# Kernel tuning notes

Hardware: AMD Instinct MI355X
Metric: run time of the kernel (lower is better)

The kernel has to match this reference:

```python
import jax, jax.numpy as jnp
import numpy as np

N_QUBITS = 8
N_LAYERS = 2
DIM = 2 ** N_QUBITS  # 256


def _ry(theta):
    h = theta * 0.5
    c, s = jnp.cos(h), jnp.sin(h)
    return jnp.stack([jnp.stack([c, -s]), jnp.stack([s, c])]).astype(jnp.complex64)


def _rz(theta):
    e = jnp.exp(-0.5j * theta.astype(jnp.complex64))
    z = jnp.zeros((), jnp.complex64)
    return jnp.stack([jnp.stack([e, z]), jnp.stack([z, jnp.conj(e)])])


def _apply_1q(state, U, w):
    # state: (2,)*n tensor, wire 0 = most significant (PennyLane convention)
    s = jnp.moveaxis(state, w, 0)
    s = jnp.tensordot(U, s, axes=((1,), (0,)))
    return jnp.moveaxis(s, 0, w)


def _cnot(state, c, t):
    s = jnp.moveaxis(state, (c, t), (0, 1))
    s = jnp.stack([s[0, 0], s[0, 1], s[1, 1], s[1, 0]]).reshape((2, 2) + s.shape[2:])
    return jnp.moveaxis(s, (0, 1), (c, t))


def _conv_pair(state, q1, q2, p):
    state = _apply_1q(state, _ry(p[0]), q1)
    state = _apply_1q(state, _ry(p[1]), q2)
    state = _cnot(state, q1, q2)
    state = _apply_1q(state, _ry(p[2]), q1)
    state = _apply_1q(state, _ry(p[3]), q2)
    state = _cnot(state, q2, q1)
    return state


def _circuit(angles, node_idx, adj, qp):
    n = N_QUBITS
    state = jnp.zeros((2,) * n, jnp.complex64).at[(0,) * n].set(1.0)
    a = jnp.clip(angles, -np.pi, np.pi)
    # angle encoding: RY on all wires, RZ on wires 0..n/2-1
    for i in range(n):
        state = _apply_1q(state, _ry(a[i]), i)
    for i in range(n // 2):
        state = _apply_1q(state, _rz(a[i + n // 2]), i)
    # graph-structure entanglement: conditional CNOT(c=node%n, t) if adj[c,t]>0
    c = (node_idx % n).astype(jnp.int32)
    adj_row = adj[c]
    flat = state.reshape(-1)
    idx = jnp.arange(DIM, dtype=jnp.int32)
    bit_c = (idx >> (n - 1 - c)) & 1  # dynamic control wire
    for t in range(n):
        perm = idx ^ (bit_c << (n - 1 - t))
        cond = (adj_row[t] > 0) & (t != c)
        flat = jnp.where(cond, flat[perm], flat)
    state = flat.reshape((2,) * n)
    # quantum conv layers
    ppc = 4 * (n - 1)
    off = 0
    for _ in range(N_LAYERS):
        p = qp[off:off + ppc]
        k = 0
        for i in range(0, n - 1, 2):
            state = _conv_pair(state, i, i + 1, p[k:k + 4]); k += 4
        for i in range(1, n - 1, 2):
            state = _conv_pair(state, i, i + 1, p[k:k + 4]); k += 4
        off += ppc
    # pooling rotations on even wires
    pool = qp[off:off + n]
    for q in range(0, n, 2):
        state = _apply_1q(state, _ry(pool[q]), q)
    # <Z_w> expectation values
    probs = jnp.abs(state) ** 2
    z = jnp.stack([probs.take(0, axis=w).sum() - probs.take(1, axis=w).sum()
                   for w in range(n)])
    return z


def setup_inputs() -> dict:
    key = jax.random.key(0)
    ks = jax.random.split(key, 12)
    B, S, N, F = 64, 12, 207, 2
    x = jax.random.normal(ks[0], (B, S, N, F), jnp.float32)
    adj = jax.random.randint(ks[1], (N, N), 0, 2).astype(jnp.float32)
    w_proj = jax.random.normal(ks[2], (N_QUBITS, S * F), jnp.float32) * 0.1
    b_proj = jax.random.normal(ks[3], (N_QUBITS,), jnp.float32) * 0.1
    q_params = jax.random.normal(ks[4], (4 * (N_QUBITS - 1) * N_LAYERS + N_QUBITS,), jnp.float32) * 0.1
    w1 = jax.random.normal(ks[5], (64, N_QUBITS), jnp.float32) * 0.1
    b1 = jax.random.normal(ks[6], (64,), jnp.float32) * 0.1
    w2 = jax.random.normal(ks[7], (32, 64), jnp.float32) * 0.1
    b2 = jax.random.normal(ks[8], (32,), jnp.float32) * 0.1
    w3 = jax.random.normal(ks[9], (1, 32), jnp.float32) * 0.1
    b3 = jax.random.normal(ks[10], (1,), jnp.float32) * 0.1
    return dict(x=x, adj=adj, w_proj=w_proj, b_proj=b_proj, q_params=q_params,
                w1=w1, b1=b1, w2=w2, b2=b2, w3=w3, b3=b3)


def reference(x, adj, w_proj, b_proj, q_params, w1, b1, w2, b2, w3, b3):
    B, S, N, F = x.shape
    feats = jnp.transpose(x, (0, 2, 1, 3)).reshape(B, N, S * F)
    angles = feats @ w_proj.T + b_proj                      # (B, N, 8)
    node_idx = jnp.tile(jnp.arange(N, dtype=jnp.int32), B)  # (B*N,)
    z = jax.vmap(_circuit, in_axes=(0, 0, None, None))(
        angles.reshape(B * N, N_QUBITS), node_idx, adj, q_params)
    # original detaches quantum features before the classical head
    z = jax.lax.stop_gradient(z).reshape(B, N, N_QUBITS).astype(jnp.float32)
    h = jax.nn.relu(z @ w1.T + b1)   # dropout is identity in eval mode
    h = jax.nn.relu(h @ w2.T + b2)
    out = h @ w3.T + b3              # (B, N, 1)
    return out.squeeze(-1)
```

## Files before the change

kernel.cpp:

```cpp
#include <hip/hip_runtime.h>
#include <math.h>

#define DEV static __device__ __forceinline__

constexpr int SS = 12;
constexpr int NN = 207;
constexpr int NCIRC = 64 * NN;


typedef float v2f __attribute__((ext_vector_type(2)));

DEV v2f splat2(float x) { v2f r; r.x = x; r.y = x; return r; }
DEV v2f vfma(float m, v2f a, v2f acc) { return __builtin_elementwise_fma(splat2(m), a, acc); }
DEV v2f vmul(float m, v2f a) { return splat2(m) * a; }
template<int M> DEV float sxc(float v) { return __shfl_xor(v, M, 64); }
template<int M> DEV v2f sx2(v2f v) { v2f r; r.x = sxc<M>(v.x); r.y = sxc<M>(v.y); return r; }

#define CONVM(P) do {                                                     \
    v2f _a0 = c0, _a1 = c1, _a2 = c2, _a3 = c3;                           \
    c0 = vfma((P)[0],  _a0, vfma((P)[1],  _a1, vfma((P)[2],  _a2, vmul((P)[3],  _a3)))); \
    c1 = vfma((P)[4],  _a0, vfma((P)[5],  _a1, vfma((P)[6],  _a2, vmul((P)[7],  _a3)))); \
    c2 = vfma((P)[8],  _a0, vfma((P)[9],  _a1, vfma((P)[10], _a2, vmul((P)[11], _a3)))); \
    c3 = vfma((P)[12], _a0, vfma((P)[13], _a1, vfma((P)[14], _a2, vmul((P)[15], _a3)))); \
} while (0)

#define SWKL1(J) do { const bool _lb = (lane >> (J)) & 1;                 \
    v2f _t0 = sx2<(1<<(J))>(c2), _t1 = sx2<(1<<(J))>(c3);                 \
    v2f _t2 = sx2<(1<<(J))>(c0), _t3 = sx2<(1<<(J))>(c1);                 \
    c0 = _lb ? _t0 : c0; c1 = _lb ? _t1 : c1;                             \
    c2 = _lb ? c2 : _t2; c3 = _lb ? c3 : _t3; } while (0)

#define SWKL0(J) do { const bool _lb = (lane >> (J)) & 1;                 \
    v2f _t0 = sx2<(1<<(J))>(c1), _t1 = sx2<(1<<(J))>(c0);                 \
    v2f _t2 = sx2<(1<<(J))>(c3), _t3 = sx2<(1<<(J))>(c2);                 \
    c0 = _lb ? _t0 : c0; c1 = _lb ? c1 : _t1;                             \
    c2 = _lb ? _t2 : c2; c3 = _lb ? c3 : _t3; } while (0)

#define RYL(J, cc_, ss_) do { const float _c = (cc_), _s = (ss_);         \
    const float _sg = ((lane >> (J)) & 1) ? _s : -_s;                     \
    v2f _p;                                                               \
    _p = sx2<(1<<(J))>(c0); c0 = __builtin_elementwise_fma(splat2(_c), c0, vmul(_sg, _p)); \
    _p = sx2<(1<<(J))>(c1); c1 = __builtin_elementwise_fma(splat2(_c), c1, vmul(_sg, _p)); \
    _p = sx2<(1<<(J))>(c2); c2 = __builtin_elementwise_fma(splat2(_c), c2, vmul(_sg, _p)); \
    _p = sx2<(1<<(J))>(c3); c3 = __builtin_elementwise_fma(splat2(_c), c3, vmul(_sg, _p)); \
} while (0)

__global__ void prep_kernel(const float* __restrict__ qp, float* __restrict__ ws) {
    const int n = threadIdx.x;
    if (n == 14) {
        float s, c;
        sincosf(0.5f * qp[56], &s, &c); ws[224] = c; ws[225] = s;
        sincosf(0.5f * qp[58], &s, &c); ws[226] = c; ws[227] = s;
        sincosf(0.5f * qp[60], &s, &c); ws[228] = c; ws[229] = s;
    }
    if (n >= 14) return;
    const int Jt[14] = {12, 8, 24, 4, 20, 0, 16, 32, 28, 44, 36, 48, 40, 52};
    const int Vt[14] = { 0, 0,  1, 0,  1, 0,  1,  0,  0,  1,  0,  1,  0,  1};
    const int J = Jt[n], v = Vt[n];
    float cg[4], sg[4];
    for (int i = 0; i < 4; i++) sincosf(0.5f * qp[J + i], &sg[i], &cg[i]);
    const int h1i = v ? 1 : 0, l1i = v ? 0 : 1;
    const int h2i = v ? 3 : 2, l2i = v ? 2 : 3;
    float A[16], B[16], M[16];
    {
        float H[2][2] = {{cg[h1i], -sg[h1i]}, {sg[h1i], cg[h1i]}};
        float L[2][2] = {{cg[l1i], -sg[l1i]}, {sg[l1i], cg[l1i]}};
        for (int a = 0; a < 2; a++) for (int b = 0; b < 2; b++)
            for (int p = 0; p < 2; p++) for (int q = 0; q < 2; q++)
                A[(2*a+b)*4 + (2*p+q)] = H[a][p] * L[b][q];
    }
    {
        const int ra = v ? 1 : 2;
        for (int j = 0; j < 4; j++) { float t = A[ra*4+j]; A[ra*4+j] = A[12+j]; A[12+j] = t; }
    }
    {
        float H[2][2] = {{cg[h2i], -sg[h2i]}, {sg[h2i], cg[h2i]}};
        float L[2][2] = {{cg[l2i], -sg[l2i]}, {sg[l2i], cg[l2i]}};
        for (int a = 0; a < 2; a++) for (int b = 0; b < 2; b++)
            for (int p = 0; p < 2; p++) for (int q = 0; q < 2; q++)
                B[(2*a+b)*4 + (2*p+q)] = H[a][p] * L[b][q];
    }
    for (int r = 0; r < 4; r++)
        for (int cl = 0; cl < 4; cl++) {
            float acc = 0.0f;
            for (int k = 0; k < 4; k++) acc += B[r*4+k] * A[k*4+cl];
            M[r*4+cl] = acc;
        }
    {
        const int rb = v ? 2 : 1;
        for (int j = 0; j < 4; j++) { float t = M[rb*4+j]; M[rb*4+j] = M[12+j]; M[12+j] = t; }
    }
    if (n == 13) {
        float ps, pc;
        sincosf(0.5f * qp[62], &ps, &pc);
        for (int j = 0; j < 4; j++) {
            float r0 = M[j],     r2 = M[8+j];
            M[j]     = pc * r0 - ps * r2;
            M[8+j]   = ps * r0 + pc * r2;
            float r1 = M[4+j],   r3 = M[12+j];
            M[4+j]   = pc * r1 - ps * r3;
            M[12+j]  = ps * r1 + pc * r3;
        }
    }
    for (int i = 0; i < 16; i++) ws[16*n + i] = M[i];
}

__global__ __launch_bounds__(256) void qcnn_kernel(
    const float* __restrict__ x, const float* __restrict__ adj,
    const float* __restrict__ w_proj, const float* __restrict__ b_proj,
    const float* __restrict__ ws,
    const float* __restrict__ w1, const float* __restrict__ b1,
    const float* __restrict__ w2, const float* __restrict__ b2,
    const float* __restrict__ w3, const float* __restrict__ b3,
    float* __restrict__ out)
{
    const int lane = threadIdx.x & 63;
    const int wv   = threadIdx.x >> 6;
    const int g    = blockIdx.x * 4 + wv;
    const int b    = g / NN;
    const int node = g - b * NN;

    v2f av[8];
#pragma unroll
    for (int k = 0; k < 8; k++) av[k] = splat2(0.0f);
    const float* xp = x + ((size_t)b * SS * NN + node) * 2;
#pragma unroll
    for (int s = 0; s < SS; s++) {
        const v2f xv = *(const v2f*)(xp + (size_t)s * (NN * 2));
#pragma unroll
        for (int k = 0; k < 8; k++) {
            const v2f wv2 = *(const v2f*)(w_proj + k * 24 + 2 * s);
            av[k] = __builtin_elementwise_fma(xv, wv2, av[k]);
        }
    }
    const float PI_F = 3.14159265358979323846f;
    float ang[8];
#pragma unroll
    for (int k = 0; k < 8; k++)
        ang[k] = fminf(fmaxf(av[k].x + av[k].y + b_proj[k], -PI_F), PI_F);

    float cc[8], ss[8];
#pragma unroll
    for (int i = 0; i < 8; i++) __sincosf(0.5f * ang[i], &ss[i], &cc[i]);

    float A = 1.0f;
#pragma unroll
    for (int i = 0; i < 6; i++)
        A *= ((lane >> (5 - i)) & 1) ? ss[i] : cc[i];
    float phi = 0.0f;
#pragma unroll
    for (int i = 0; i < 4; i++)
        phi += ((lane >> (5 - i)) & 1) ? 0.5f * ang[4 + i] : -0.5f * ang[4 + i];
    float cp, sp;
    __sincosf(phi, &sp, &cp);

    v2f ph; ph.x = cp; ph.y = sp;
    v2f c0 = vmul(A * cc[6] * cc[7], ph);
    v2f c1 = vmul(A * cc[6] * ss[7], ph);
    v2f c2 = vmul(A * ss[6] * cc[7], ph);
    v2f c3 = vmul(A * ss[6] * ss[7], ph);

    const int cq = node & 7;
    int M = 0;
#pragma unroll
    for (int t = 0; t < 8; t++) {
        float avv = adj[cq * NN + t];
        if (t != cq && avv > 0.0f) M |= 1 << (7 - t);
    }
    if (M) {
        const int Mlane = M >> 2;
        const int Mlo   = M & 3;
        v2f p0, p1, p2, p3;
        if (Mlo == 0)      { p0 = c0; p1 = c1; p2 = c2; p3 = c3; }
        else if (Mlo == 1) { p0 = c1; p1 = c0; p2 = c3; p3 = c2; }
        else if (Mlo == 2) { p0 = c2; p1 = c3; p2 = c0; p3 = c1; }
        else               { p0 = c3; p1 = c2; p2 = c1; p3 = c0; }
        p0.x = __shfl_xor(p0.x, Mlane, 64); p0.y = __shfl_xor(p0.y, Mlane, 64);
        p1.x = __shfl_xor(p1.x, Mlane, 64); p1.y = __shfl_xor(p1.y, Mlane, 64);
        p2.x = __shfl_xor(p2.x, Mlane, 64); p2.y = __shfl_xor(p2.y, Mlane, 64);
        p3.x = __shfl_xor(p3.x, Mlane, 64); p3.y = __shfl_xor(p3.y, Mlane, 64);
        const int pc = 7 - cq;
        if (pc >= 2) {
            const bool bb = (lane >> (pc - 2)) & 1;
            c0 = bb ? p0 : c0; c1 = bb ? p1 : c1;
            c2 = bb ? p2 : c2; c3 = bb ? p3 : c3;
        } else if (pc == 1) {
            c2 = p2; c3 = p3;
        } else {
            c1 = p1; c3 = p3;
        }
    }

    CONVM(ws + 0);
    SWKL1(1);
    SWKL0(0);
    CONVM(ws + 16);
    SWKL1(1);
    CONVM(ws + 32);
    SWKL1(3);
    SWKL0(2);
    CONVM(ws + 48);
    SWKL1(1);
    CONVM(ws + 64);
    SWKL1(5);
    SWKL0(4);
    CONVM(ws + 80);
    SWKL1(1);
    CONVM(ws + 96);
    SWKL0(4);
    CONVM(ws + 112);
    SWKL1(1);
    SWKL0(4);
    CONVM(ws + 128);
    SWKL1(1);
    CONVM(ws + 144);
    SWKL1(5);
    SWKL0(2);
    CONVM(ws + 160);
    SWKL0(4);
    CONVM(ws + 176);
    SWKL1(3);
    SWKL0(0);
    CONVM(ws + 192);
    SWKL0(4);
    CONVM(ws + 208);

    RYL(1, ws[224], ws[225]);
    RYL(5, ws[226], ws[227]);
    RYL(3, ws[228], ws[229]);

    const float p0 = fmaf(c0.x, c0.x, c0.y * c0.y);
    const float p1 = fmaf(c1.x, c1.x, c1.y * c1.y);
    const float p2 = fmaf(c2.x, c2.x, c2.y * c2.y);
    const float p3 = fmaf(c3.x, c3.x, c3.y * c3.y);
    const float psum = (p0 + p1) + (p2 + p3);
    const float zK1 = (p0 + p1) - (p2 + p3);
    const float zK0 = (p0 - p1) + (p2 - p3);
    v2f za, zb, zc, zd;
    za.x = ((lane >> 1) & 1) ? -psum : psum;
    za.y = ((lane >> 2) & 1) ? -psum : psum;
    zb.x = ((lane >> 5) & 1) ? -psum : psum;
    zb.y = (lane & 1)        ? -psum : psum;
    zc.x = ((lane >> 3) & 1) ? -psum : psum;
    zc.y = zK0;
    zd.x = zK1;
    zd.y = ((lane >> 4) & 1) ? -psum : psum;

#define BFLY(MM) do { za += sx2<MM>(za); zb += sx2<MM>(zb);               \
                      zc += sx2<MM>(zc); zd += sx2<MM>(zd); } while (0)
    BFLY(1); BFLY(2); BFLY(4); BFLY(8); BFLY(16); BFLY(32);
#undef BFLY

    const v2f* w1v = (const v2f*)(w1 + lane * 8);
    v2f hv = za * w1v[0];
    hv = __builtin_elementwise_fma(zb, w1v[1], hv);
    hv = __builtin_elementwise_fma(zc, w1v[2], hv);
    hv = __builtin_elementwise_fma(zd, w1v[3], hv);
    const float h1 = fmaxf(b1[lane] + hv.x + hv.y, 0.0f);

    __shared__ float h1s[4][64];
    h1s[wv][lane] = h1;
    __syncthreads();

    const int m = lane & 31;
    const v2f* w2v = (const v2f*)(w2 + m * 64);
    const v2f* hsv = (const v2f*)(&h1s[wv][0]);
    v2f acc2 = splat2(0.0f);
#pragma unroll
    for (int j = 0; j < 32; j++)
        acc2 = __builtin_elementwise_fma(hsv[j], w2v[j], acc2);
    const float h2 = fmaxf(b2[m] + acc2.x + acc2.y, 0.0f);

    float o = h2 * w3[m];
    o += sxc<1>(o);
    o += sxc<2>(o);
    o += sxc<4>(o);
    o += sxc<8>(o);
    o += sxc<16>(o);

    if (lane == 0) out[g] = o + b3[0];
}

extern "C" void kernel_launch(void* const* d_in, const int* in_sizes, int n_in,
                              void* d_out, int out_size, void* d_ws, size_t ws_size,
                              hipStream_t stream) {
    const float* x      = (const float*)d_in[0];
    const float* adj    = (const float*)d_in[1];
    const float* w_proj = (const float*)d_in[2];
    const float* b_proj = (const float*)d_in[3];
    const float* qp     = (const float*)d_in[4];
    const float* w1     = (const float*)d_in[5];
    const float* b1     = (const float*)d_in[6];
    const float* w2     = (const float*)d_in[7];
    const float* b2     = (const float*)d_in[8];
    const float* w3     = (const float*)d_in[9];
    const float* b3     = (const float*)d_in[10];
    float* out = (float*)d_out;
    float* ws  = (float*)d_ws;

    hipLaunchKernelGGL(prep_kernel, dim3(1), dim3(64), 0, stream, qp, ws);
    hipLaunchKernelGGL(qcnn_kernel, dim3(NCIRC / 4), dim3(256), 0, stream,
                       x, adj, w_proj, b_proj, ws, w1, b1, w2, b2, w3, b3, out);
}
```

Baseline: 115.0 us.

## Process two circuits per wavefront to share constants and add ILP

Each wavefront now simulates two circuits, the same node in batches b and b+32, with interleaved state updates. The grid is halved. The circuit code is moved into helper functions, and the adjacency mask, the ws conv matrices and the w1 weights are loaded once and used for both states. Interleaving two independent shuffle/FMA chains is meant to hide cross-lane shuffle latency and amortise the uniform loads. The cost is higher register pressure, and the barrier before the per-wave shared-memory MLP stage is removed.

```diff
diff --git a/kernel.cpp b/kernel.cpp
--- a/kernel.cpp
+++ b/kernel.cpp
@@ -6,6 +6,7 @@
 constexpr int SS = 12;
 constexpr int NN = 207;
 constexpr int NCIRC = 64 * NN;
+constexpr int NPAIR = NCIRC / 2;
 
 
 typedef float v2f __attribute__((ext_vector_type(2)));
@@ -16,34 +17,124 @@
 template<int M> DEV float sxc(float v) { return __shfl_xor(v, M, 64); }
 template<int M> DEV v2f sx2(v2f v) { v2f r; r.x = sxc<M>(v.x); r.y = sxc<M>(v.y); return r; }
 
-#define CONVM(P) do {                                                     \
-    v2f _a0 = c0, _a1 = c1, _a2 = c2, _a3 = c3;                           \
-    c0 = vfma((P)[0],  _a0, vfma((P)[1],  _a1, vfma((P)[2],  _a2, vmul((P)[3],  _a3)))); \
-    c1 = vfma((P)[4],  _a0, vfma((P)[5],  _a1, vfma((P)[6],  _a2, vmul((P)[7],  _a3)))); \
-    c2 = vfma((P)[8],  _a0, vfma((P)[9],  _a1, vfma((P)[10], _a2, vmul((P)[11], _a3)))); \
-    c3 = vfma((P)[12], _a0, vfma((P)[13], _a1, vfma((P)[14], _a2, vmul((P)[15], _a3)))); \
-} while (0)
-
-#define SWKL1(J) do { const bool _lb = (lane >> (J)) & 1;                 \
-    v2f _t0 = sx2<(1<<(J))>(c2), _t1 = sx2<(1<<(J))>(c3);                 \
-    v2f _t2 = sx2<(1<<(J))>(c0), _t3 = sx2<(1<<(J))>(c1);                 \
-    c0 = _lb ? _t0 : c0; c1 = _lb ? _t1 : c1;                             \
-    c2 = _lb ? c2 : _t2; c3 = _lb ? c3 : _t3; } while (0)
-
-#define SWKL0(J) do { const bool _lb = (lane >> (J)) & 1;                 \
-    v2f _t0 = sx2<(1<<(J))>(c1), _t1 = sx2<(1<<(J))>(c0);                 \
-    v2f _t2 = sx2<(1<<(J))>(c3), _t3 = sx2<(1<<(J))>(c2);                 \
-    c0 = _lb ? _t0 : c0; c1 = _lb ? c1 : _t1;                             \
-    c2 = _lb ? _t2 : c2; c3 = _lb ? c3 : _t3; } while (0)
-
-#define RYL(J, cc_, ss_) do { const float _c = (cc_), _s = (ss_);         \
-    const float _sg = ((lane >> (J)) & 1) ? _s : -_s;                     \
-    v2f _p;                                                               \
-    _p = sx2<(1<<(J))>(c0); c0 = __builtin_elementwise_fma(splat2(_c), c0, vmul(_sg, _p)); \
-    _p = sx2<(1<<(J))>(c1); c1 = __builtin_elementwise_fma(splat2(_c), c1, vmul(_sg, _p)); \
-    _p = sx2<(1<<(J))>(c2); c2 = __builtin_elementwise_fma(splat2(_c), c2, vmul(_sg, _p)); \
-    _p = sx2<(1<<(J))>(c3); c3 = __builtin_elementwise_fma(splat2(_c), c3, vmul(_sg, _p)); \
-} while (0)
+struct Ct { v2f a0, a1, a2, a3; };
+
+DEV void convm(Ct& s, const float* __restrict__ P) {
+    v2f b0 = s.a0, b1 = s.a1, b2 = s.a2, b3 = s.a3;
+    s.a0 = vfma(P[0],  b0, vfma(P[1],  b1, vfma(P[2],  b2, vmul(P[3],  b3))));
+    s.a1 = vfma(P[4],  b0, vfma(P[5],  b1, vfma(P[6],  b2, vmul(P[7],  b3))));
+    s.a2 = vfma(P[8],  b0, vfma(P[9],  b1, vfma(P[10], b2, vmul(P[11], b3))));
+    s.a3 = vfma(P[12], b0, vfma(P[13], b1, vfma(P[14], b2, vmul(P[15], b3))));
+}
+
+template<int J> DEV void swkl1(Ct& s, int lane) {
+    const bool lb = (lane >> J) & 1;
+    v2f t0 = sx2<(1 << J)>(s.a2), t1 = sx2<(1 << J)>(s.a3);
+    v2f t2 = sx2<(1 << J)>(s.a0), t3 = sx2<(1 << J)>(s.a1);
+    s.a0 = lb ? t0 : s.a0; s.a1 = lb ? t1 : s.a1;
+    s.a2 = lb ? s.a2 : t2; s.a3 = lb ? s.a3 : t3;
+}
+
+template<int J> DEV void swkl0(Ct& s, int lane) {
+    const bool lb = (lane >> J) & 1;
+    v2f t0 = sx2<(1 << J)>(s.a1), t1 = sx2<(1 << J)>(s.a0);
+    v2f t2 = sx2<(1 << J)>(s.a3), t3 = sx2<(1 << J)>(s.a2);
+    s.a0 = lb ? t0 : s.a0; s.a1 = lb ? s.a1 : t1;
+    s.a2 = lb ? t2 : s.a2; s.a3 = lb ? s.a3 : t3;
+}
+
+template<int J> DEV void ryl(Ct& s, int lane, float c, float sv) {
+    const float sg = ((lane >> J) & 1) ? sv : -sv;
+    v2f p;
+    p = sx2<(1 << J)>(s.a0); s.a0 = __builtin_elementwise_fma(splat2(c), s.a0, vmul(sg, p));
+    p = sx2<(1 << J)>(s.a1); s.a1 = __builtin_elementwise_fma(splat2(c), s.a1, vmul(sg, p));
+    p = sx2<(1 << J)>(s.a2); s.a2 = __builtin_elementwise_fma(splat2(c), s.a2, vmul(sg, p));
+    p = sx2<(1 << J)>(s.a3); s.a3 = __builtin_elementwise_fma(splat2(c), s.a3, vmul(sg, p));
+}
+
+DEV Ct init_state(const float* __restrict__ xp, const float* __restrict__ w_proj,
+                  const float* __restrict__ b_proj, int lane) {
+    v2f av[8];
+#pragma unroll
+    for (int k = 0; k < 8; k++) av[k] = splat2(0.0f);
+#pragma unroll
+    for (int s = 0; s < SS; s++) {
+        const v2f xv = *(const v2f*)(xp + (size_t)s * (NN * 2));
+#pragma unroll
+        for (int k = 0; k < 8; k++) {
+            const v2f wv2 = *(const v2f*)(w_proj + k * 24 + 2 * s);
+            av[k] = __builtin_elementwise_fma(xv, wv2, av[k]);
+        }
+    }
+    const float PI_F = 3.14159265358979323846f;
+    float ang[8];
+#pragma unroll
+    for (int k = 0; k < 8; k++)
+        ang[k] = fminf(fmaxf(av[k].x + av[k].y + b_proj[k], -PI_F), PI_F);
+    float cc[8], ssn[8];
+#pragma unroll
+    for (int i = 0; i < 8; i++) __sincosf(0.5f * ang[i], &ssn[i], &cc[i]);
+    float A = 1.0f;
+#pragma unroll
+    for (int i = 0; i < 6; i++)
+        A *= ((lane >> (5 - i)) & 1) ? ssn[i] : cc[i];
+    float phi = 0.0f;
+#pragma unroll
+    for (int i = 0; i < 4; i++)
+        phi += ((lane >> (5 - i)) & 1) ? 0.5f * ang[4 + i] : -0.5f * ang[4 + i];
+    float cp, sp;
+    __sincosf(phi, &sp, &cp);
+    v2f ph; ph.x = cp; ph.y = sp;
+    Ct s;
+    s.a0 = vmul(A * cc[6] * cc[7], ph);
+    s.a1 = vmul(A * cc[6] * ssn[7], ph);
+    s.a2 = vmul(A * ssn[6] * cc[7], ph);
+    s.a3 = vmul(A * ssn[6] * ssn[7], ph);
+    return s;
+}
+
+DEV Ct adj_gather(const Ct& s, int Mlane, int Mlo) {
+    v2f p0, p1, p2, p3;
+    if (Mlo == 0)      { p0 = s.a0; p1 = s.a1; p2 = s.a2; p3 = s.a3; }
+    else if (Mlo == 1) { p0 = s.a1; p1 = s.a0; p2 = s.a3; p3 = s.a2; }
+    else if (Mlo == 2) { p0 = s.a2; p1 = s.a3; p2 = s.a0; p3 = s.a1; }
+    else               { p0 = s.a3; p1 = s.a2; p2 = s.a1; p3 = s.a0; }
+    p0.x = __shfl_xor(p0.x, Mlane, 64); p0.y = __shfl_xor(p0.y, Mlane, 64);
+    p1.x = __shfl_xor(p1.x, Mlane, 64); p1.y = __shfl_xor(p1.y, Mlane, 64);
+    p2.x = __shfl_xor(p2.x, Mlane, 64); p2.y = __shfl_xor(p2.y, Mlane, 64);
+    p3.x = __shfl_xor(p3.x, Mlane, 64); p3.y = __shfl_xor(p3.y, Mlane, 64);
+    Ct r; r.a0 = p0; r.a1 = p1; r.a2 = p2; r.a3 = p3;
+    return r;
+}
+
+DEV void adj_select(Ct& s, const Ct& p, int pc, int lane) {
+    if (pc >= 2) {
+        const bool bb = (lane >> (pc - 2)) & 1;
+        s.a0 = bb ? p.a0 : s.a0; s.a1 = bb ? p.a1 : s.a1;
+        s.a2 = bb ? p.a2 : s.a2; s.a3 = bb ? p.a3 : s.a3;
+    } else if (pc == 1) { s.a2 = p.a2; s.a3 = p.a3; }
+    else                { s.a1 = p.a1; s.a3 = p.a3; }
+}
+
+DEV void build_z(const Ct& s, int lane, v2f& za, v2f& zb, v2f& zc, v2f& zd) {
+    const float p0 = fmaf(s.a0.x, s.a0.x, s.a0.y * s.a0.y);
+    const float p1 = fmaf(s.a1.x, s.a1.x, s.a1.y * s.a1.y);
+    const float p2 = fmaf(s.a2.x, s.a2.x, s.a2.y * s.a2.y);
+    const float p3 = fmaf(s.a3.x, s.a3.x, s.a3.y * s.a3.y);
+    const float psum = (p0 + p1) + (p2 + p3);
+    za.x = ((lane >> 1) & 1) ? -psum : psum;
+    za.y = ((lane >> 2) & 1) ? -psum : psum;
+    zb.x = ((lane >> 5) & 1) ? -psum : psum;
+    zb.y = (lane & 1)        ? -psum : psum;
+    zc.x = ((lane >> 3) & 1) ? -psum : psum;
+    zc.y = (p0 - p1) + (p2 - p3);
+    zd.x = (p0 + p1) - (p2 + p3);
+    zd.y = ((lane >> 4) & 1) ? -psum : psum;
+#define BFLY(MM) do { za += sx2<MM>(za); zb += sx2<MM>(zb);               \
+                      zc += sx2<MM>(zc); zd += sx2<MM>(zd); } while (0)
+    BFLY(1); BFLY(2); BFLY(4); BFLY(8); BFLY(16); BFLY(32);
+#undef BFLY
+}
 
 __global__ void prep_kernel(const float* __restrict__ qp, float* __restrict__ ws) {
     const int n = threadIdx.x;
@@ -69,10 +160,8 @@
             for (int p = 0; p < 2; p++) for (int q = 0; q < 2; q++)
                 A[(2*a+b)*4 + (2*p+q)] = H[a][p] * L[b][q];
     }
-    {
-        const int ra = v ? 1 : 2;
-        for (int j = 0; j < 4; j++) { float t = A[ra*4+j]; A[ra*4+j] = A[12+j]; A[12+j] = t; }
-    }
+    { const int ra = v ? 1 : 2;
+      for (int j = 0; j < 4; j++) { float t = A[ra*4+j]; A[ra*4+j] = A[12+j]; A[12+j] = t; } }
     {
         float H[2][2] = {{cg[h2i], -sg[h2i]}, {sg[h2i], cg[h2i]}};
         float L[2][2] = {{cg[l2i], -sg[l2i]}, {sg[l2i], cg[l2i]}};
@@ -86,20 +175,16 @@
             for (int k = 0; k < 4; k++) acc += B[r*4+k] * A[k*4+cl];
             M[r*4+cl] = acc;
         }
-    {
-        const int rb = v ? 2 : 1;
-        for (int j = 0; j < 4; j++) { float t = M[rb*4+j]; M[rb*4+j] = M[12+j]; M[12+j] = t; }
-    }
+    { const int rb = v ? 2 : 1;
+      for (int j = 0; j < 4; j++) { float t = M[rb*4+j]; M[rb*4+j] = M[12+j]; M[12+j] = t; } }
     if (n == 13) {
         float ps, pc;
         sincosf(0.5f * qp[62], &ps, &pc);
         for (int j = 0; j < 4; j++) {
-            float r0 = M[j],     r2 = M[8+j];
-            M[j]     = pc * r0 - ps * r2;
-            M[8+j]   = ps * r0 + pc * r2;
-            float r1 = M[4+j],   r3 = M[12+j];
-            M[4+j]   = pc * r1 - ps * r3;
-            M[12+j]  = ps * r1 + pc * r3;
+            float r0 = M[j],   r2 = M[8+j];
+            M[j]   = pc * r0 - ps * r2;  M[8+j]  = ps * r0 + pc * r2;
+            float r1 = M[4+j], r3 = M[12+j];
+            M[4+j] = pc * r1 - ps * r3;  M[12+j] = ps * r1 + pc * r3;
         }
     }
     for (int i = 0; i < 16; i++) ws[16*n + i] = M[i];
@@ -116,49 +201,16 @@
 {
     const int lane = threadIdx.x & 63;
     const int wv   = threadIdx.x >> 6;
-    const int g    = blockIdx.x * 4 + wv;
-    const int b    = g / NN;
-    const int node = g - b * NN;
-
-    v2f av[8];
-#pragma unroll
-    for (int k = 0; k < 8; k++) av[k] = splat2(0.0f);
-    const float* xp = x + ((size_t)b * SS * NN + node) * 2;
-#pragma unroll
-    for (int s = 0; s < SS; s++) {
-        const v2f xv = *(const v2f*)(xp + (size_t)s * (NN * 2));
-#pragma unroll
-        for (int k = 0; k < 8; k++) {
-            const v2f wv2 = *(const v2f*)(w_proj + k * 24 + 2 * s);
-            av[k] = __builtin_elementwise_fma(xv, wv2, av[k]);
-        }
-    }
-    const float PI_F = 3.14159265358979323846f;
-    float ang[8];
-#pragma unroll
-    for (int k = 0; k < 8; k++)
-        ang[k] = fminf(fmaxf(av[k].x + av[k].y + b_proj[k], -PI_F), PI_F);
-
-    float cc[8], ss[8];
-#pragma unroll
-    for (int i = 0; i < 8; i++) __sincosf(0.5f * ang[i], &ss[i], &cc[i]);
-
-    float A = 1.0f;
-#pragma unroll
-    for (int i = 0; i < 6; i++)
-        A *= ((lane >> (5 - i)) & 1) ? ss[i] : cc[i];
-    float phi = 0.0f;
-#pragma unroll
-    for (int i = 0; i < 4; i++)
-        phi += ((lane >> (5 - i)) & 1) ? 0.5f * ang[4 + i] : -0.5f * ang[4 + i];
-    float cp, sp;
-    __sincosf(phi, &sp, &cp);
-
-    v2f ph; ph.x = cp; ph.y = sp;
-    v2f c0 = vmul(A * cc[6] * cc[7], ph);
-    v2f c1 = vmul(A * cc[6] * ss[7], ph);
-    v2f c2 = vmul(A * ss[6] * cc[7], ph);
-    v2f c3 = vmul(A * ss[6] * ss[7], ph);
+    const int gA   = blockIdx.x * 4 + wv;
+    const int gB   = gA + NPAIR;
+    const int bA   = gA / NN;
+    const int node = gA - bA * NN;
+
+    const float* xpA = x + ((size_t)bA * SS * NN + node) * 2;
+    const float* xpB = xpA + (size_t)32 * SS * NN * 2;
+
+    Ct sA = init_state(xpA, w_proj, b_proj, lane);
+    Ct sB = init_state(xpB, w_proj, b_proj, lane);
 
     const int cq = node & 7;
     int M = 0;
@@ -168,103 +220,76 @@
         if (t != cq && avv > 0.0f) M |= 1 << (7 - t);
     }
     if (M) {
-        const int Mlane = M >> 2;
-        const int Mlo   = M & 3;
-        v2f p0, p1, p2, p3;
-        if (Mlo == 0)      { p0 = c0; p1 = c1; p2 = c2; p3 = c3; }
-        else if (Mlo == 1) { p0 = c1; p1 = c0; p2 = c3; p3 = c2; }
-        else if (Mlo == 2) { p0 = c2; p1 = c3; p2 = c0; p3 = c1; }
-        else               { p0 = c3; p1 = c2; p2 = c1; p3 = c0; }
-        p0.x = __shfl_xor(p0.x, Mlane, 64); p0.y = __shfl_xor(p0.y, Mlane, 64);
-        p1.x = __shfl_xor(p1.x, Mlane, 64); p1.y = __shfl_xor(p1.y, Mlane, 64);
-        p2.x = __shfl_xor(p2.x, Mlane, 64); p2.y = __shfl_xor(p2.y, Mlane, 64);
-        p3.x = __shfl_xor(p3.x, Mlane, 64); p3.y = __shfl_xor(p3.y, Mlane, 64);
-        const int pc = 7 - cq;
-        if (pc >= 2) {
-            const bool bb = (lane >> (pc - 2)) & 1;
-            c0 = bb ? p0 : c0; c1 = bb ? p1 : c1;
-            c2 = bb ? p2 : c2; c3 = bb ? p3 : c3;
-        } else if (pc == 1) {
-            c2 = p2; c3 = p3;
-        } else {
-            c1 = p1; c3 = p3;
-        }
-    }
-
-    CONVM(ws + 0);
-    SWKL1(1);
-    SWKL0(0);
-    CONVM(ws + 16);
-    SWKL1(1);
-    CONVM(ws + 32);
-    SWKL1(3);
-    SWKL0(2);
-    CONVM(ws + 48);
-    SWKL1(1);
-    CONVM(ws + 64);
-    SWKL1(5);
-    SWKL0(4);
-    CONVM(ws + 80);
-    SWKL1(1);
-    CONVM(ws + 96);
-    SWKL0(4);
-    CONVM(ws + 112);
-    SWKL1(1);
-    SWKL0(4);
-    CONVM(ws + 128);
-    SWKL1(1);
-    CONVM(ws + 144);
-    SWKL1(5);
-    SWKL0(2);
-    CONVM(ws + 160);
-    SWKL0(4);
-    CONVM(ws + 176);
-    SWKL1(3);
-    SWKL0(0);
-    CONVM(ws + 192);
-    SWKL0(4);
-    CONVM(ws + 208);
-
-    RYL(1, ws[224], ws[225]);
-    RYL(5, ws[226], ws[227]);
-    RYL(3, ws[228], ws[229]);
-
-    const float p0 = fmaf(c0.x, c0.x, c0.y * c0.y);
-    const float p1 = fmaf(c1.x, c1.x, c1.y * c1.y);
-    const float p2 = fmaf(c2.x, c2.x, c2.y * c2.y);
-    const float p3 = fmaf(c3.x, c3.x, c3.y * c3.y);
-    const float psum = (p0 + p1) + (p2 + p3);
-    const float zK1 = (p0 + p1) - (p2 + p3);
-    const float zK0 = (p0 - p1) + (p2 - p3);
-    v2f za, zb, zc, zd;
-    za.x = ((lane >> 1) & 1) ? -psum : psum;
-    za.y = ((lane >> 2) & 1) ? -psum : psum;
-    zb.x = ((lane >> 5) & 1) ? -psum : psum;
-    zb.y = (lane & 1)        ? -psum : psum;
-    zc.x = ((lane >> 3) & 1) ? -psum : psum;
-    zc.y = zK0;
-    zd.x = zK1;
-    zd.y = ((lane >> 4) & 1) ? -psum : psum;
-
-#define BFLY(MM) do { za += sx2<MM>(za); zb += sx2<MM>(zb);               \
-                      zc += sx2<MM>(zc); zd += sx2<MM>(zd); } while (0)
-    BFLY(1); BFLY(2); BFLY(4); BFLY(8); BFLY(16); BFLY(32);
-#undef BFLY
+        const int Mlane = M >> 2, Mlo = M & 3, pc = 7 - cq;
+        Ct pA = adj_gather(sA, Mlane, Mlo);
+        Ct pB = adj_gather(sB, Mlane, Mlo);
+        adj_select(sA, pA, pc, lane);
+        adj_select(sB, pB, pc, lane);
+    }
+
+#define C2(OFF)  do { convm(sA, ws + (OFF)); convm(sB, ws + (OFF)); } while (0)
+#define S12(J)   do { swkl1<J>(sA, lane); swkl1<J>(sB, lane); } while (0)
+#define S02(J)   do { swkl0<J>(sA, lane); swkl0<J>(sB, lane); } while (0)
+    C2(0);
+    S12(1); S02(0);
+    C2(16);
+    S12(1);
+    C2(32);
+    S12(3); S02(2);
+    C2(48);
+    S12(1);
+    C2(64);
+    S12(5); S02(4);
+    C2(80);
+    S12(1);
+    C2(96);
+    S02(4);
+    C2(112);
+    S12(1); S02(4);
+    C2(128);
+    S12(1);
+    C2(144);
+    S12(5); S02(2);
+    C2(160);
+    S02(4);
+    C2(176);
+    S12(3); S02(0);
+    C2(192);
+    S02(4);
+    C2(208);
+#undef C2
+#undef S12
+#undef S02
+
+    ryl<1>(sA, lane, ws[224], ws[225]); ryl<1>(sB, lane, ws[224], ws[225]);
+    ryl<5>(sA, lane, ws[226], ws[227]); ryl<5>(sB, lane, ws[226], ws[227]);
+    ryl<3>(sA, lane, ws[228], ws[229]); ryl<3>(sB, lane, ws[228], ws[229]);
+
+    v2f zaA, zbA, zcA, zdA, zaB, zbB, zcB, zdB;
+    build_z(sA, lane, zaA, zbA, zcA, zdA);
+    build_z(sB, lane, zaB, zbB, zcB, zdB);
 
     const v2f* w1v = (const v2f*)(w1 + lane * 8);
-    v2f hv = za * w1v[0];
-    hv = __builtin_elementwise_fma(zb, w1v[1], hv);
-    hv = __builtin_elementwise_fma(zc, w1v[2], hv);
-    hv = __builtin_elementwise_fma(zd, w1v[3], hv);
-    const float h1 = fmaxf(b1[lane] + hv.x + hv.y, 0.0f);
-
-    __shared__ float h1s[4][64];
-    h1s[wv][lane] = h1;
-    __syncthreads();
+    const v2f w10 = w1v[0], w11 = w1v[1], w12 = w1v[2], w13 = w1v[3];
+    v2f hA = zaA * w10;
+    hA = __builtin_elementwise_fma(zbA, w11, hA);
+    hA = __builtin_elementwise_fma(zcA, w12, hA);
+    hA = __builtin_elementwise_fma(zdA, w13, hA);
+    v2f hB = zaB * w10;
+    hB = __builtin_elementwise_fma(zbB, w11, hB);
+    hB = __builtin_elementwise_fma(zcB, w12, hB);
+    hB = __builtin_elementwise_fma(zdB, w13, hB);
+    const float bb1 = b1[lane];
+    const float h1A = fmaxf(bb1 + hA.x + hA.y, 0.0f);
+    const float h1B = fmaxf(bb1 + hB.x + hB.y, 0.0f);
+
+    __shared__ float h1s[8][64];
+    h1s[2 * wv][lane]     = h1A;
+    h1s[2 * wv + 1][lane] = h1B;
 
     const int m = lane & 31;
+    const v2f* hsv = (const v2f*)(&h1s[2 * wv + (lane >> 5)][0]);
     const v2f* w2v = (const v2f*)(w2 + m * 64);
-    const v2f* hsv = (const v2f*)(&h1s[wv][0]);
     v2f acc2 = splat2(0.0f);
 #pragma unroll
     for (int j = 0; j < 32; j++)
@@ -272,13 +297,9 @@
     const float h2 = fmaxf(b2[m] + acc2.x + acc2.y, 0.0f);
 
     float o = h2 * w3[m];
-    o += sxc<1>(o);
-    o += sxc<2>(o);
-    o += sxc<4>(o);
-    o += sxc<8>(o);
-    o += sxc<16>(o);
-
-    if (lane == 0) out[g] = o + b3[0];
+    o += sxc<1>(o); o += sxc<2>(o); o += sxc<4>(o); o += sxc<8>(o); o += sxc<16>(o);
+
+    if (m == 0) out[(lane >> 5) ? gB : gA] = o + b3[0];
 }
 
 extern "C" void kernel_launch(void* const* d_in, const int* in_sizes, int n_in,
@@ -299,6 +320,6 @@
     float* ws  = (float*)d_ws;
 
     hipLaunchKernelGGL(prep_kernel, dim3(1), dim3(64), 0, stream, qp, ws);
-    hipLaunchKernelGGL(qcnn_kernel, dim3(NCIRC / 4), dim3(256), 0, stream,
+    hipLaunchKernelGGL(qcnn_kernel, dim3(NPAIR / 4), dim3(256), 0, stream,
                        x, adj, w_proj, b_proj, ws, w1, b1, w2, b2, w3, b3, out);
 }
```

Result: slower. 117.6 us (+2.3%).
